# Optimization experiments

Measured on AMD Instinct MI355X. Metric: run time of the kernel, lower is better.

Reference implementation:

```python
import jax, jax.numpy as jnp
import numpy as np

N, D, H = 3072, 1152, 16
HD = D // H  # 72


def setup_inputs() -> dict:
    key = jax.random.key(0)
    ks = jax.random.split(key, 12)
    w = lambda k, shp: jax.random.normal(k, shp, dtype=jnp.float32) * 0.02
    return {
        "hidden_states": jax.random.normal(ks[0], (N, D), dtype=jnp.float32),
        "rotary_pos_emb": jax.random.normal(ks[1], (N, HD // 2), dtype=jnp.float32),
        "cu_seqlens": jnp.arange(5, dtype=jnp.int32) * (N // 4),
        "wq": w(ks[2], (D, D)), "bq": jnp.zeros((D,), jnp.float32),
        "wk": w(ks[3], (D, D)), "bk": jnp.zeros((D,), jnp.float32),
        "wv": w(ks[4], (D, D)), "bv": jnp.zeros((D,), jnp.float32),
        "wo": w(ks[5], (D, D)), "bo": jnp.zeros((D,), jnp.float32),
    }


def _rotate_half(x):
    x1, x2 = jnp.split(x, 2, axis=-1)
    return jnp.concatenate((-x2, x1), axis=-1)


def _apply_rope(t, freqs):
    # t: [N, H, HD], freqs: [N, HD//2]
    cos = jnp.concatenate([jnp.cos(freqs), jnp.cos(freqs)], axis=-1)[:, None, :]  # [N,1,HD]
    sin = jnp.concatenate([jnp.sin(freqs), jnp.sin(freqs)], axis=-1)[:, None, :]
    return (t.astype(jnp.float32) * cos + _rotate_half(t.astype(jnp.float32)) * sin).astype(t.dtype)


def reference(hidden_states, rotary_pos_emb, cu_seqlens, wq, bq, wk, bk, wv, bv, wo, bo):
    n = hidden_states.shape[0]
    q = (hidden_states @ wq.T + bq).reshape(n, H, HD)
    k = (hidden_states @ wk.T + bk).reshape(n, H, HD)
    v = (hidden_states @ wv.T + bv).reshape(n, H, HD)
    q = _apply_rope(q, rotary_pos_emb)
    k = _apply_rope(k, rotary_pos_emb)
    # block-diagonal mask: same segment id (from cu_seqlens) -> attend
    seg = jnp.searchsorted(cu_seqlens, jnp.arange(n), side="right")
    same = seg[:, None] == seg[None, :]  # [N, N]
    neg = jnp.finfo(q.dtype).min
    scores = jnp.einsum("qhd,khd->hqk", q, k) / jnp.sqrt(jnp.float32(HD)).astype(q.dtype)
    scores = scores + jnp.where(same, jnp.zeros((), q.dtype), neg)[None, :, :]
    attn = jax.nn.softmax(scores.astype(jnp.float32), axis=-1).astype(q.dtype)
    out = jnp.einsum("hqk,khd->qhd", attn, v).reshape(n, D)
    return out @ wo.T + bo
```

## Files before the change

### kernel.cpp

```cpp
#include <hip/hip_runtime.h>
#include <hip/hip_bf16.h>


typedef __attribute__((ext_vector_type(8))) __bf16 bf16x8;
typedef __attribute__((ext_vector_type(4))) float f32x4;
typedef __attribute__((ext_vector_type(8))) unsigned short u16x8;
typedef __attribute__((ext_vector_type(4))) unsigned short u16x4;

#define N_TOK 3072
#define DMODEL 1152
#define NH 16
#define HDIM 72
#define SEGLEN 768

__device__ __forceinline__ unsigned short bf16rn(float f) {
  union { float f; unsigned int u; } v; v.f = f;
  return (unsigned short)((v.u + 0x7fffu + ((v.u >> 16) & 1u)) >> 16);
}
__device__ __forceinline__ float bf2f(unsigned short u) {
  union { unsigned int i; float f; } v; v.i = ((unsigned int)u) << 16;
  return v.f;
}

#define GLOAD16(gsrc, ldst)                                                  \
  __builtin_amdgcn_global_load_lds(                                         \
      (const __attribute__((address_space(1))) unsigned int*)(gsrc),        \
      (__attribute__((address_space(3))) unsigned int*)(ldst), 16, 0, 0)

__global__ __launch_bounds__(256) void prep_kernel(
    const float* __restrict__ hs,
    const float* __restrict__ wq, const float* __restrict__ wk,
    const float* __restrict__ wv, const float* __restrict__ wo,
    const float* __restrict__ bq, const float* __restrict__ bk,
    const float* __restrict__ bv,
    unsigned short* __restrict__ Xbf, unsigned short* __restrict__ Wqkv,
    unsigned short* __restrict__ Wo, float* __restrict__ biasqkv) {
  const int idx = blockIdx.x * 256 + threadIdx.x;
  const int stride = gridDim.x * 256;
  const int NX4 = (N_TOK * DMODEL) / 4;
  const int NW4 = (DMODEL * DMODEL) / 4;
  for (int i = idx; i < NX4; i += stride) {
    f32x4 v = ((const f32x4*)hs)[i];
    u16x4 o;
    for (int j = 0; j < 4; ++j) o[j] = bf16rn(v[j]);
    ((u16x4*)Xbf)[i] = o;
  }
  for (int i = idx; i < NW4; i += stride) {
    f32x4 a = ((const f32x4*)wq)[i];
    f32x4 b = ((const f32x4*)wk)[i];
    f32x4 c = ((const f32x4*)wv)[i];
    f32x4 d = ((const f32x4*)wo)[i];
    u16x4 oa, ob, oc, od;
    for (int j = 0; j < 4; ++j) {
      oa[j] = bf16rn(a[j]); ob[j] = bf16rn(b[j]);
      oc[j] = bf16rn(c[j]); od[j] = bf16rn(d[j]);
    }
    ((u16x4*)Wqkv)[i] = oa;
    ((u16x4*)(Wqkv + DMODEL * DMODEL))[i] = ob;
    ((u16x4*)(Wqkv + 2 * DMODEL * DMODEL))[i] = oc;
    ((u16x4*)Wo)[i] = od;
  }
  for (int i = idx; i < DMODEL; i += stride) {
    biasqkv[i] = bq[i];
    biasqkv[DMODEL + i] = bk[i];
    biasqkv[2 * DMODEL + i] = bv[i];
  }
}

template <int BM, int BN, int FM, int FN, bool OBF>
__global__ __launch_bounds__(256) void gemm_lds_kernel(
    const unsigned short* __restrict__ A, const unsigned short* __restrict__ B,
    const float* __restrict__ bias, void* __restrict__ Cout,
    int Nout, int K, int nbx) {
  __shared__ unsigned short As[2][BM * 32];
  __shared__ unsigned short Bs[2][BN * 32];
  const int t = threadIdx.x;
  const int lane = t & 63, wave = t >> 6;
  const int wr = wave >> 1, wc = wave & 1;
  const int g = lane >> 4, li = lane & 15;

  const int per = gridDim.x >> 3;
  const int gb = (blockIdx.x & 7) * per + (blockIdx.x >> 3);
  const int by = gb / nbx, bx = gb - by * nbx;
  const int bm = by * BM, bn = bx * BN;

  constexpr int LA = BM / 64;
  constexpr int LB = BN / 64;

  auto stage = [&](int buf, int kt) {
#pragma unroll
    for (int i = 0; i < LA; ++i) {
      const int s = i * 256 + t;
      const int row = s >> 2, cs = s & 3;
      const int gg = cs ^ ((row >> 1) & 3);
      GLOAD16(A + (long)(bm + row) * K + kt + gg * 8,
              &As[buf][(i * 256 + (t & ~63)) * 8]);
    }
#pragma unroll
    for (int i = 0; i < LB; ++i) {
      const int s = i * 256 + t;
      const int row = s >> 2, cs = s & 3;
      const int gg = cs ^ ((row >> 1) & 3);
      GLOAD16(B + (long)(bn + row) * K + kt + gg * 8,
              &Bs[buf][(i * 256 + (t & ~63)) * 8]);
    }
  };

  f32x4 acc[FM][FN];
#pragma unroll
  for (int i = 0; i < FM; ++i)
#pragma unroll
    for (int j = 0; j < FN; ++j) acc[i][j] = (f32x4)0.f;

  stage(0, 0);
  int cur = 0;
  const int nk = K / 32;
  for (int kt = 0; kt < nk; ++kt) {
    __syncthreads();
    if (kt + 1 < nk) stage(cur ^ 1, (kt + 1) * 32);
    bf16x8 af[FM], bf[FN];
#pragma unroll
    for (int i = 0; i < FM; ++i) {
      const int r = wr * (BM / 2) + i * 16 + li;
      af[i] = *(const bf16x8*)&As[cur][r * 32 + ((g ^ ((r >> 1) & 3)) * 8)];
    }
#pragma unroll
    for (int j = 0; j < FN; ++j) {
      const int r = wc * (BN / 2) + j * 16 + li;
      bf[j] = *(const bf16x8*)&Bs[cur][r * 32 + ((g ^ ((r >> 1) & 3)) * 8)];
    }
#pragma unroll
    for (int i = 0; i < FM; ++i)
#pragma unroll
      for (int j = 0; j < FN; ++j)
        acc[i][j] = __builtin_amdgcn_mfma_f32_16x16x32_bf16(af[i], bf[j],
                                                            acc[i][j], 0, 0, 0);
    cur ^= 1;
  }

#pragma unroll
  for (int i = 0; i < FM; ++i) {
    const int row = bm + wr * (BM / 2) + i * 16 + g * 4;
#pragma unroll
    for (int j = 0; j < FN; ++j) {
      const int col = bn + wc * (BN / 2) + j * 16 + li;
      const float bb = bias[col];
#pragma unroll
      for (int r = 0; r < 4; ++r) {
        const float v = acc[i][j][r] + bb;
        if constexpr (OBF)
          ((unsigned short*)Cout)[(long)(row + r) * Nout + col] = bf16rn(v);
        else
          ((float*)Cout)[(long)(row + r) * Nout + col] = v;
      }
    }
  }
}

__global__ __launch_bounds__(256) void rope_pack_kernel(
    const unsigned short* __restrict__ qkv, const float* __restrict__ rope,
    unsigned short* __restrict__ Qp, unsigned short* __restrict__ Kp,
    unsigned short* __restrict__ Vt) {
  const int nb = blockIdx.x;
  const int h = blockIdx.y;
  const int n0 = nb * 64;
  const int t = threadIdx.x;
  const float qscale = 0.11785113f;
  __shared__ float cs[64][36], sn[64][36];
  __shared__ float vtile[72][65];

  for (int i = t; i < 64 * 36; i += 256) {
    const int n = i / 36, d = i % 36;
    const float f = rope[(long)(n0 + n) * 36 + d];
    cs[n][d] = __cosf(f);
    sn[n][d] = __sinf(f);
  }
  __syncthreads();

  for (int i = t; i < 64 * 9; i += 256) {
    const int n = i / 9, dq = (i % 9) * 4;
    const long base = (long)(n0 + n) * 3456 + h * HDIM;
    u16x4 q1 = *(const u16x4*)&qkv[base + dq];
    u16x4 q2 = *(const u16x4*)&qkv[base + dq + 36];
    u16x4 k1 = *(const u16x4*)&qkv[base + DMODEL + dq];
    u16x4 k2 = *(const u16x4*)&qkv[base + DMODEL + dq + 36];
    u16x4 oq1, oq2, ok1, ok2;
#pragma unroll
    for (int e = 0; e < 4; ++e) {
      const float c = cs[n][dq + e], s = sn[n][dq + e];
      float f1 = bf2f(q1[e]), f2 = bf2f(q2[e]);
      oq1[e] = bf16rn((f1 * c - f2 * s) * qscale);
      oq2[e] = bf16rn((f2 * c + f1 * s) * qscale);
      f1 = bf2f(k1[e]); f2 = bf2f(k2[e]);
      ok1[e] = bf16rn(f1 * c - f2 * s);
      ok2[e] = bf16rn(f2 * c + f1 * s);
    }
    const long ob = ((long)h * N_TOK + n0 + n) * 96;
    *(u16x4*)&Qp[ob + dq] = oq1;
    *(u16x4*)&Qp[ob + dq + 36] = oq2;
    *(u16x4*)&Kp[ob + dq] = ok1;
    *(u16x4*)&Kp[ob + dq + 36] = ok2;
  }
  for (int i = t; i < 64 * 6; i += 256) {
    const int n = i / 6, dp = HDIM + (i % 6) * 4;
    const long ob = ((long)h * N_TOK + n0 + n) * 96;
    *(u16x4*)&Qp[ob + dp] = (u16x4)0;
    *(u16x4*)&Kp[ob + dp] = (u16x4)0;
  }
  for (int i = t; i < 64 * 9; i += 256) {
    const int n = i / 9, dq = (i % 9) * 8;
    u16x8 v = *(const u16x8*)&qkv[(long)(n0 + n) * 3456 + 2 * DMODEL + h * HDIM + dq];
#pragma unroll
    for (int e = 0; e < 8; ++e) vtile[dq + e][n] = bf2f(v[e]);
  }
  __syncthreads();
  for (int i = t; i < 80 * 8; i += 256) {
    const int d = i / 8, nq = (i % 8) * 8;
    u16x8 o;
#pragma unroll
    for (int e = 0; e < 8; ++e)
      o[e] = (d < HDIM) ? bf16rn(vtile[d][nq + e]) : (unsigned short)0;
    *(u16x8*)&Vt[((long)h * 80 + d) * N_TOK + n0 + nq] = o;
  }
}

__global__ __launch_bounds__(256) void attn_kernel(
    const unsigned short* __restrict__ Qp, const unsigned short* __restrict__ Kp,
    const unsigned short* __restrict__ Vt, unsigned short* __restrict__ pO,
    float* __restrict__ pl) {
  const int b = blockIdx.x;
  const int hs = b & 63, u = b >> 6;
  const int h = hs >> 2, seg = hs & 3;
  const int qt = u >> 1, half = u & 1;
  const int t = threadIdx.x;
  const int lane = t & 63, w = t >> 6;
  const int g = lane >> 4, li = lane & 15;

  __shared__ unsigned short Ks[2][32 * 96];
  __shared__ unsigned short Vs[2][80 * 32];
  __shared__ unsigned short Ps[4][16][40];

  const int q0 = seg * SEGLEN + qt * 64;
  const int koff0 = half * 384;
  const unsigned short* kbase = Kp + ((long)h * N_TOK + seg * SEGLEN) * 96;
  const unsigned short* vbase = Vt + (long)h * 80 * N_TOK + seg * SEGLEN;

  auto stageK = [&](int buf, int koff) {
    {
      const int row = t / 12, c = t - row * 12;
      const int gg = c ^ ((row >> 1) & 3);
      GLOAD16(kbase + (long)(koff + row) * 96 + gg * 8,
              &Ks[buf][(t & ~63) * 8]);
    }
    if (t < 128) {
      const int s = 256 + t;
      const int row = s / 12, c = s - row * 12;
      const int gg = c ^ ((row >> 1) & 3);
      GLOAD16(kbase + (long)(koff + row) * 96 + gg * 8,
              &Ks[buf][(256 + (t & ~63)) * 8]);
    }
  };
  auto stageV = [&](int buf, int koff) {
    {
      const int row = t >> 2, ch = t & 3;
      const int gg = ch ^ ((row >> 1) & 3);
      GLOAD16(vbase + (long)row * N_TOK + koff + gg * 8,
              &Vs[buf][(t & ~63) * 8]);
    }
    if (t < 64) {
      const int s = 256 + t;
      const int row = s >> 2, ch = s & 3;
      const int gg = ch ^ ((row >> 1) & 3);
      GLOAD16(vbase + (long)row * N_TOK + koff + gg * 8,
              &Vs[buf][(256 + (t & ~63)) * 8]);
    }
  };

  bf16x8 aq[3];
  {
    const unsigned short* qsrc = Qp + ((long)h * N_TOK + q0 + w * 16 + li) * 96;
#pragma unroll
    for (int c = 0; c < 3; ++c)
      aq[c] = *(const bf16x8*)(qsrc + c * 32 + g * 8);
  }

  f32x4 accO[5];
#pragma unroll
  for (int j = 0; j < 5; ++j) accO[j] = (f32x4)0.f;
  float l[4] = {0.f, 0.f, 0.f, 0.f};

  stageK(0, koff0);
  stageV(0, koff0);
  int cur = 0;
  for (int kv = 0; kv < 12; ++kv) {
    __syncthreads();
    if (kv + 1 < 12) {
      stageK(cur ^ 1, koff0 + (kv + 1) * 32);
      stageV(cur ^ 1, koff0 + (kv + 1) * 32);
    }

    f32x4 sc[2];
#pragma unroll
    for (int f = 0; f < 2; ++f) sc[f] = (f32x4)0.f;
#pragma unroll
    for (int c = 0; c < 3; ++c)
#pragma unroll
      for (int f = 0; f < 2; ++f) {
        const int kr = f * 16 + li;
        bf16x8 bk = *(const bf16x8*)
            &Ks[cur][kr * 96 + (((c * 4 + g) ^ ((kr >> 1) & 3)) * 8)];
        sc[f] = __builtin_amdgcn_mfma_f32_16x16x32_bf16(aq[c], bk, sc[f], 0, 0, 0);
      }

#pragma unroll
    for (int r = 0; r < 4; ++r) {
      float p0 = __expf(sc[0][r]);
      float p1 = __expf(sc[1][r]);
      float rs = p0 + p1;
      rs += __shfl_xor(rs, 1);
      rs += __shfl_xor(rs, 2);
      rs += __shfl_xor(rs, 4);
      rs += __shfl_xor(rs, 8);
      l[r] += rs;
      Ps[w][g * 4 + r][li] = bf16rn(p0);
      Ps[w][g * 4 + r][16 + li] = bf16rn(p1);
    }

    {
      bf16x8 ap = *(const bf16x8*)&Ps[w][li][g * 8];
#pragma unroll
      for (int j = 0; j < 5; ++j) {
        const int vr = j * 16 + li;
        bf16x8 bv = *(const bf16x8*)
            &Vs[cur][vr * 32 + ((g ^ ((vr >> 1) & 3)) * 8)];
        accO[j] = __builtin_amdgcn_mfma_f32_16x16x32_bf16(ap, bv, accO[j], 0, 0, 0);
      }
    }
    cur ^= 1;
  }

  const long pbase = ((long)(half * 16 + h)) * N_TOK;
#pragma unroll
  for (int j = 0; j < 5; ++j) {
    const int d = j * 16 + li;
#pragma unroll
    for (int r = 0; r < 4; ++r) {
      const int n = q0 + w * 16 + g * 4 + r;
      pO[(pbase + n) * 80 + d] = bf16rn(accO[j][r]);
    }
  }
  if (li == 0) {
#pragma unroll
    for (int r = 0; r < 4; ++r)
      pl[pbase + q0 + w * 16 + g * 4 + r] = l[r];
  }
}

__global__ __launch_bounds__(256) void combine_kernel(
    const unsigned short* __restrict__ pO, const float* __restrict__ pl,
    unsigned short* __restrict__ AO) {
  const int idx = blockIdx.x * 256 + threadIdx.x;
  const int row = idx / 9, q = idx - row * 9;
  const long HS = (long)NH * N_TOK * 80;
  u16x8 a = *(const u16x8*)&pO[(long)row * 80 + q * 8];
  u16x8 b = *(const u16x8*)&pO[HS + (long)row * 80 + q * 8];
  const float linv = 1.f / (pl[row] + pl[NH * N_TOK + row]);
  const int h = row / N_TOK, n = row - h * N_TOK;
  u16x8 o;
#pragma unroll
  for (int e = 0; e < 8; ++e)
    o[e] = bf16rn((bf2f(a[e]) + bf2f(b[e])) * linv);
  *(u16x8*)&AO[(long)n * DMODEL + h * HDIM + q * 8] = o;
}

extern "C" void kernel_launch(void* const* d_in, const int* in_sizes, int n_in,
                              void* d_out, int out_size, void* d_ws,
                              size_t ws_size, hipStream_t stream) {
  const float* hs = (const float*)d_in[0];
  const float* rope = (const float*)d_in[1];
  const float* wq = (const float*)d_in[3];
  const float* bq = (const float*)d_in[4];
  const float* wk = (const float*)d_in[5];
  const float* bk = (const float*)d_in[6];
  const float* wv = (const float*)d_in[7];
  const float* bv = (const float*)d_in[8];
  const float* wo = (const float*)d_in[9];
  const float* bo = (const float*)d_in[10];
  float* out = (float*)d_out;
  char* ws = (char*)d_ws;

  unsigned short* Xbf = (unsigned short*)(ws + 0);
  unsigned short* Wqkv = (unsigned short*)(ws + 7077888);
  unsigned short* Wo = (unsigned short*)(ws + 15040512);
  float* biasqkv = (float*)(ws + 17694720);
  unsigned short* qkvb = (unsigned short*)(ws + 17708544);
  unsigned short* pO = (unsigned short*)(ws + 17708544);
  float* pl = (float*)(ws + 33437184);
  unsigned short* Qp = (unsigned short*)(ws + 38942208);
  unsigned short* Kp = (unsigned short*)(ws + 48379392);
  unsigned short* Vt = (unsigned short*)(ws + 57816576);
  unsigned short* AO = (unsigned short*)(ws + 65680896);

  prep_kernel<<<dim3(1024), dim3(256), 0, stream>>>(
      hs, wq, wk, wv, wo, bq, bk, bv, Xbf, Wqkv, Wo, biasqkv);
  gemm_lds_kernel<128, 128, 4, 4, true><<<dim3(648), dim3(256), 0, stream>>>(
      Xbf, Wqkv, biasqkv, qkvb, 3 * DMODEL, DMODEL, 27);
  rope_pack_kernel<<<dim3(48, 16), dim3(256), 0, stream>>>(
      qkvb, rope, Qp, Kp, Vt);
  attn_kernel<<<dim3(1536), dim3(256), 0, stream>>>(Qp, Kp, Vt, pO, pl);
  combine_kernel<<<dim3(1728), dim3(256), 0, stream>>>(pO, pl, AO);
  gemm_lds_kernel<64, 128, 2, 4, false><<<dim3(432), dim3(256), 0, stream>>>(
      AO, Wo, bo, out, DMODEL, DMODEL, 9);
}
```

Before: 125.8 us.

## Fold softmax row-sum into PV MFMA via ones column, use exp2 and setprio

```diff
diff --git a/kernel.cpp b/kernel.cpp
--- a/kernel.cpp
+++ b/kernel.cpp
@@ -129,12 +129,14 @@
       const int r = wc * (BN / 2) + j * 16 + li;
       bf[j] = *(const bf16x8*)&Bs[cur][r * 32 + ((g ^ ((r >> 1) & 3)) * 8)];
     }
+    __builtin_amdgcn_s_setprio(1);
 #pragma unroll
     for (int i = 0; i < FM; ++i)
 #pragma unroll
       for (int j = 0; j < FN; ++j)
         acc[i][j] = __builtin_amdgcn_mfma_f32_16x16x32_bf16(af[i], bf[j],
                                                             acc[i][j], 0, 0, 0);
+    __builtin_amdgcn_s_setprio(0);
     cur ^= 1;
   }
 
@@ -165,7 +167,7 @@
   const int h = blockIdx.y;
   const int n0 = nb * 64;
   const int t = threadIdx.x;
-  const float qscale = 0.11785113f;
+  const float qscale = 0.17002501f;
   __shared__ float cs[64][36], sn[64][36];
   __shared__ float vtile[72][65];
 
@@ -219,7 +221,9 @@
     u16x8 o;
 #pragma unroll
     for (int e = 0; e < 8; ++e)
-      o[e] = (d < HDIM) ? bf16rn(vtile[d][nq + e]) : (unsigned short)0;
+      o[e] = (d < HDIM) ? bf16rn(vtile[d][nq + e])
+                        : (d == HDIM ? (unsigned short)0x3F80
+                                     : (unsigned short)0);
     *(u16x8*)&Vt[((long)h * 80 + d) * N_TOK + n0 + nq] = o;
   }
 }
@@ -238,7 +242,7 @@
 
   __shared__ unsigned short Ks[2][32 * 96];
   __shared__ unsigned short Vs[2][80 * 32];
-  __shared__ unsigned short Ps[4][16][40];
+  __shared__ unsigned short Ps[4][16][48];
 
   const int q0 = seg * SEGLEN + qt * 64;
   const int koff0 = half * 384;
@@ -287,7 +291,6 @@
   f32x4 accO[5];
 #pragma unroll
   for (int j = 0; j < 5; ++j) accO[j] = (f32x4)0.f;
-  float l[4] = {0.f, 0.f, 0.f, 0.f};
 
   stageK(0, koff0);
   stageV(0, koff0);
@@ -302,6 +305,7 @@
     f32x4 sc[2];
 #pragma unroll
     for (int f = 0; f < 2; ++f) sc[f] = (f32x4)0.f;
+    __builtin_amdgcn_s_setprio(1);
 #pragma unroll
     for (int c = 0; c < 3; ++c)
 #pragma unroll
@@ -309,25 +313,21 @@
         const int kr = f * 16 + li;
         bf16x8 bk = *(const bf16x8*)
             &Ks[cur][kr * 96 + (((c * 4 + g) ^ ((kr >> 1) & 3)) * 8)];
-        sc[f] = __builtin_amdgcn_mfma_f32_16x16x32_bf16(aq[c], bk, sc[f], 0, 0, 0);
+        sc[f] = __builtin_amdgcn_mfma_f32_16x16x32_bf16(bk, aq[c], sc[f], 0, 0, 0);
       }
-
-#pragma unroll
-    for (int r = 0; r < 4; ++r) {
-      float p0 = __expf(sc[0][r]);
-      float p1 = __expf(sc[1][r]);
-      float rs = p0 + p1;
-      rs += __shfl_xor(rs, 1);
-      rs += __shfl_xor(rs, 2);
-      rs += __shfl_xor(rs, 4);
-      rs += __shfl_xor(rs, 8);
-      l[r] += rs;
-      Ps[w][g * 4 + r][li] = bf16rn(p0);
-      Ps[w][g * 4 + r][16 + li] = bf16rn(p1);
+    __builtin_amdgcn_s_setprio(0);
+
+#pragma unroll
+    for (int f = 0; f < 2; ++f) {
+      u16x4 pk;
+#pragma unroll
+      for (int r = 0; r < 4; ++r) pk[r] = bf16rn(exp2f(sc[f][r]));
+      *(u16x4*)&Ps[w][li][f * 16 + g * 4] = pk;
     }
 
     {
       bf16x8 ap = *(const bf16x8*)&Ps[w][li][g * 8];
+      __builtin_amdgcn_s_setprio(1);
 #pragma unroll
       for (int j = 0; j < 5; ++j) {
         const int vr = j * 16 + li;
@@ -335,6 +335,7 @@
             &Vs[cur][vr * 32 + ((g ^ ((vr >> 1) & 3)) * 8)];
         accO[j] = __builtin_amdgcn_mfma_f32_16x16x32_bf16(ap, bv, accO[j], 0, 0, 0);
       }
+      __builtin_amdgcn_s_setprio(0);
     }
     cur ^= 1;
   }
@@ -349,10 +350,10 @@
       pO[(pbase + n) * 80 + d] = bf16rn(accO[j][r]);
     }
   }
-  if (li == 0) {
+  if (li == 8) {
 #pragma unroll
     for (int r = 0; r < 4; ++r)
-      pl[pbase + q0 + w * 16 + g * 4 + r] = l[r];
+      pl[pbase + q0 + w * 16 + g * 4 + r] = accO[4][r];
   }
 }
 
```

New measurement: 116.8 us. -7.2%, faster.
